# Performance work log

Measured on AMD Instinct MI355X. Metric: run time of the kernel, lower is better.

The kernel has to match this reference:

```python
import jax, jax.numpy as jnp
import numpy as np

BN_EPS = 1e-5
ITER_N = 5

def _bn(x, gamma, beta, mean, var, axis):
    shape = [1] * x.ndim
    shape[axis] = -1
    r = lambda v: v.reshape(shape)
    return (x - r(mean)) * (r(gamma) / jnp.sqrt(r(var) + BN_EPS)) + r(beta)

def _covpool(x):
    # x: (B, d, M); MPNCOV CovpoolLayer: y = x @ I_hat @ x^T, I_hat = (1/M)I - (1/M^2)11^T
    M = x.shape[-1]
    I_hat = (-1.0 / (M * M)) * jnp.ones((M, M), x.dtype) + (1.0 / M) * jnp.eye(M, dtype=x.dtype)
    return jnp.einsum('bdm,mn,ben->bde', x, I_hat, x)

def _sqrtm_ns(A, iterN=ITER_N):
    # MPNCOV SqrtmLayer: trace-normalized Newton-Schulz iteration
    d = A.shape[-1]
    I3 = 3.0 * jnp.eye(d, dtype=A.dtype)
    normA = jnp.trace(A, axis1=1, axis2=2) / 3.0          # (B,)
    A_n = A / normA[:, None, None]
    ZY = 0.5 * (I3 - A_n)
    Y = A_n @ ZY
    Z = ZY
    for _ in range(iterN - 2):
        ZY = 0.5 * (I3 - Z @ Y)
        Y = Y @ ZY
        Z = ZY @ Z
    YZY = 0.5 * (Y @ (I3 - Z @ Y))
    return YZY * jnp.sqrt(normA)[:, None, None]

def setup_inputs() -> dict:
    key = jax.random.key(0)
    ks = jax.random.split(key, 12)
    B, C, H, W = 64, 1024, 16, 16
    D, R = 128, H * W  # att_dim, sp_reso
    return {
        'x': jax.random.normal(ks[0], (B, C, H, W), jnp.float32),
        'w_dr': jax.random.normal(ks[1], (D, C), jnp.float32) * 0.02,
        'b_dr': jax.random.normal(ks[2], (D,), jnp.float32) * 0.02,
        'bn1_gamma': jnp.ones((D,), jnp.float32),
        'bn1_beta': jnp.zeros((D,), jnp.float32),
        'bn1_mean': jax.random.normal(ks[3], (D,), jnp.float32) * 0.1,
        'bn1_var': jax.random.uniform(ks[4], (D,), jnp.float32, 0.5, 1.5),
        'bn2_gamma': jnp.ones((R,), jnp.float32),
        'bn2_beta': jnp.zeros((R,), jnp.float32),
        'bn2_mean': jax.random.normal(ks[5], (R,), jnp.float32) * 0.1,
        'bn2_var': jax.random.uniform(ks[6], (R,), jnp.float32, 0.5, 1.5),
        'rc_w': jax.random.normal(ks[7], (R,), jnp.float32) * 0.1 + 1.0,
        'rc_b': jax.random.normal(ks[8], (R,), jnp.float32) * 0.02,
        'fc_w': jax.random.normal(ks[9], (R, R * R), jnp.float32) * 0.004,
        'fc_b': jax.random.normal(ks[10], (R,), jnp.float32) * 0.02,
    }

def reference(x, w_dr, b_dr, bn1_gamma, bn1_beta, bn1_mean, bn1_var,
              bn2_gamma, bn2_beta, bn2_mean, bn2_var, rc_w, rc_b, fc_w, fc_b):
    B, C, H, W = x.shape
    # 1x1 dimension-reduction conv + BN + ReLU
    y = jnp.einsum('bchw,dc->bdhw', x, w_dr) + b_dr[None, :, None, None]
    y = jax.nn.relu(_bn(y, bn1_gamma, bn1_beta, bn1_mean, bn1_var, axis=1))
    # (B, D, HW) -> (B, HW, D): HW spatial positions as 'channels', D as samples
    y = y.reshape(B, -1, H * W).transpose(0, 2, 1)
    cov = _covpool(y)                  # (B, HW, HW)
    s = _sqrtm_ns(cov, ITER_N)         # (B, HW, HW)
    # row BN over first HW axis (channels of the (B, HW, HW, 1) view)
    s = _bn(s, bn2_gamma, bn2_beta, bn2_mean, bn2_var, axis=1)
    # grouped (depthwise) 1x1 row conv: per-row scale + bias
    s = s * rc_w[None, :, None] + rc_b[None, :, None]
    att = jax.nn.sigmoid(s.reshape(B, -1) @ fc_w.T + fc_b)   # (B, HW)
    att = att.reshape(B, 1, H, W)
    return x * att
```

## Files before the change

### kernel.cpp

```cpp
#include <hip/hip_runtime.h>

typedef unsigned short u16;
typedef unsigned int   u32;
typedef __attribute__((ext_vector_type(8))) short bf8;
typedef __attribute__((ext_vector_type(4))) float f4;
typedef __attribute__((ext_vector_type(16))) float f16f;

#define MFMA(a,b,c)   __builtin_amdgcn_mfma_f32_16x16x32_bf16(a,b,c,0,0,0)
#define MFMA32(a,b,c) __builtin_amdgcn_mfma_f32_32x32x16_bf16(a,b,c,0,0,0)

__device__ __forceinline__ u16 f2bf(float f){
  u32 u = __float_as_uint(f);
  u += 0x7fffu + ((u >> 16) & 1u);
  return (u16)(u >> 16);
}
__device__ __forceinline__ float bf2f(u16 h){ return __uint_as_float(((u32)h) << 16); }
__device__ __forceinline__ u32 pk2(float a, float b){ return (u32)f2bf(a) | ((u32)f2bf(b) << 16); }

__device__ __forceinline__ void glds16(const u16* g, u16* l){
  __builtin_amdgcn_global_load_lds((const __attribute__((address_space(1))) u32*)g,
                                   (__attribute__((address_space(3))) u32*)l, 16, 0, 0);
}

__device__ __forceinline__ bf8 ldsFrag(const char* m, int row0, int k0, int pitch){
  int l = threadIdx.x & 63;
  int r = row0 + (l & 15);
  int kb = ((k0 + ((l >> 4) << 3)) << 1) ^ ((r & 7) << 4);
  return *(const bf8*)(m + r * pitch + kb);
}
__device__ __forceinline__ void ldsPut(char* m, int row, int col, int pitch, u16 v){
  int kb = (col << 1) ^ ((row & 7) << 4);
  *(u16*)(m + row * pitch + kb) = v;
}

__device__ __forceinline__ bf8 fragNS(const char* m, int r0, int ks, int l){
  int r = r0 + (l & 31);
  int kb = ((ks << 5) + ((l >> 5) << 4)) ^ ((r & 15) << 4);
  return *(const bf8*)(m + r * 256 + kb);
}
__device__ __forceinline__ bf8 fragWT(const char* m, int r0, int ks, int l){
  int r = r0 + (l & 31);
  int kb = ((ks << 5) + ((l >> 5) << 4)) ^ ((r & 15) << 4);
  return *(const bf8*)(m + r * 512 + kb);
}
__device__ __forceinline__ char* nsAddr(char* m, int row, int col4){
  return m + row * 256 + ((col4 << 1) ^ ((row & 15) << 4));
}

__device__ __forceinline__ void mmPass(const char* A, const char* B, f16f (&acc)[2][2],
                                       int R0, int C0, int l){
  #pragma unroll
  for (int ks = 0; ks < 8; ++ks){
    bf8 a0 = fragNS(A, R0,      ks, l);
    bf8 a1 = fragNS(A, R0 + 32, ks, l);
    bf8 b0 = fragNS(B, C0,      ks, l);
    bf8 b1 = fragNS(B, C0 + 32, ks, l);
    acc[0][0] = MFMA32(a0, b0, acc[0][0]); acc[0][1] = MFMA32(a0, b1, acc[0][1]);
    acc[1][0] = MFMA32(a1, b0, acc[1][0]); acc[1][1] = MFMA32(a1, b1, acc[1][1]);
  }
}

__device__ __forceinline__ void writeTile(char* D, const f16f (&acc)[2][2], int R0, int C0, int l,
                                          float scale, float dval, const uint2* adv){
  #pragma unroll
  for (int ri = 0; ri < 2; ++ri)
  #pragma unroll
  for (int ci = 0; ci < 2; ++ci)
  #pragma unroll
  for (int g = 0; g < 4; ++g){
    int srow = C0 + ci * 32 + (l & 31);
    int scol = R0 + ri * 32 + g * 8 + ((l >> 5) << 2);
    float v[4];
    #pragma unroll
    for (int q = 0; q < 4; ++q){
      float x = scale * acc[ri][ci][g * 4 + q];
      x += ((scol + q) == srow) ? dval : 0.f;
      v[q] = x;
    }
    if (adv){
      uint2 ad = adv[(ri * 2 + ci) * 4 + g];
      v[0] += 1.5f * bf2f((u16)ad.x);
      v[1] += 1.5f * bf2f((u16)(ad.x >> 16));
      v[2] += 1.5f * bf2f((u16)ad.y);
      v[3] += 1.5f * bf2f((u16)(ad.y >> 16));
    }
    *(uint2*)nsAddr(D, srow, scol) = make_uint2(pk2(v[0], v[1]), pk2(v[2], v[3]));
  }
}

__global__ __launch_bounds__(256) void k_prep(const float* __restrict__ wdr,
                                              float* __restrict__ logits,
                                              u16* __restrict__ prep){
  int i = blockIdx.x * 256 + threadIdx.x;
  if (i < 16384) logits[i] = 0.f;
  #pragma unroll
  for (int j = 0; j < 2; ++j){
    int e = i + j * 65536;
    int chunk = e >> 13, rem = e & 8191, d = rem >> 6, cb2 = rem & 63;
    int c = ((cb2 * 2) ^ ((d & 7) << 4)) >> 1;
    prep[e] = f2bf(wdr[d * 1024 + chunk * 64 + c]);
  }
}

__global__ __launch_bounds__(512) void k_conv(
    const u16* __restrict__ wprep, const float* __restrict__ x, const float* __restrict__ bdr,
    const float* __restrict__ g1, const float* __restrict__ be1,
    const float* __restrict__ m1, const float* __restrict__ v1,
    u16* __restrict__ Wg, u16* __restrict__ WTg){
  __shared__ union {
    struct { u16 A[2][8192]; u16 Bt[2][2048]; } s;
    struct { float y[128 * 33]; float musum[512]; float mu[32]; } e;
  } sm;
  int t = threadIdx.x;
  int b = blockIdx.x >> 3, hw0 = (blockIdx.x & 7) * 32;
  const float* xb = x + (size_t)b * 262144 + hw0;

  int w = t >> 6, l = t & 63;
  int d0 = (w >> 1) * 32, hh = (w & 1) * 16;
  int lc = l & 15, lr = (l >> 4) * 4;

  const f4 fz = {0.f, 0.f, 0.f, 0.f};
  f4 acc[2]; acc[0] = fz; acc[1] = fz;

  int cp = t >> 5, hwl = t & 31;
  int bo0 = (4 * cp) ^ ((hwl & 7) << 4);
  int bo1 = (4 * cp + 64) ^ ((hwl & 7) << 4);

  glds16(wprep + t * 8,        sm.s.A[0] + t * 8);
  glds16(wprep + 4096 + t * 8, sm.s.A[0] + 4096 + t * 8);
  glds16(wprep + 8192 + t * 8,        sm.s.A[1] + t * 8);
  glds16(wprep + 8192 + 4096 + t * 8, sm.s.A[1] + 4096 + t * 8);
  float br0 = xb[(size_t)(2 * cp)      * 256 + hwl];
  float br1 = xb[(size_t)(2 * cp + 1)  * 256 + hwl];
  float br2 = xb[(size_t)(2 * cp + 32) * 256 + hwl];
  float br3 = xb[(size_t)(2 * cp + 33) * 256 + hwl];

  #pragma unroll
  for (int k = 0; k < 16; ++k){
    if (k >= 1 && k < 15){
      const u16* src = wprep + (k + 1) * 8192;
      glds16(src + t * 8,        sm.s.A[(k + 1) & 1] + t * 8);
      glds16(src + 4096 + t * 8, sm.s.A[(k + 1) & 1] + 4096 + t * 8);
    }
    float nb0 = 0.f, nb1 = 0.f, nb2 = 0.f, nb3 = 0.f;
    if (k < 15){
      int c0 = (k + 1) * 64;
      nb0 = xb[(size_t)(c0 + 2 * cp)      * 256 + hwl];
      nb1 = xb[(size_t)(c0 + 2 * cp + 1)  * 256 + hwl];
      nb2 = xb[(size_t)(c0 + 2 * cp + 32) * 256 + hwl];
      nb3 = xb[(size_t)(c0 + 2 * cp + 33) * 256 + hwl];
    }
    __builtin_amdgcn_sched_barrier(0);
    if (k == 0)       asm volatile("s_waitcnt vmcnt(4)" ::: "memory");
    else if (k == 15) asm volatile("s_waitcnt vmcnt(0)" ::: "memory");
    else              asm volatile("s_waitcnt vmcnt(6)" ::: "memory");
    __builtin_amdgcn_sched_barrier(0);
    *(u32*)((char*)sm.s.Bt[k & 1] + hwl * 128 + bo0) = pk2(br0, br1);
    *(u32*)((char*)sm.s.Bt[k & 1] + hwl * 128 + bo1) = pk2(br2, br3);
    asm volatile("s_waitcnt lgkmcnt(0)" ::: "memory");
    __builtin_amdgcn_sched_barrier(0);
    __builtin_amdgcn_s_barrier();
    __builtin_amdgcn_sched_barrier(0);
    #pragma unroll
    for (int ks = 0; ks < 2; ++ks){
      int k0 = ks * 32;
      bf8 a0 = ldsFrag((const char*)sm.s.A[k & 1], d0,      k0, 128);
      bf8 a1 = ldsFrag((const char*)sm.s.A[k & 1], d0 + 16, k0, 128);
      bf8 b0 = ldsFrag((const char*)sm.s.Bt[k & 1], hh, k0, 128);
      acc[0] = MFMA(a0, b0, acc[0]);
      acc[1] = MFMA(a1, b0, acc[1]);
    }
    __builtin_amdgcn_sched_barrier(0);
    __builtin_amdgcn_s_barrier();
    __builtin_amdgcn_sched_barrier(0);
    br0 = nb0; br1 = nb1; br2 = nb2; br3 = nb3;
  }
  __syncthreads();

  #pragma unroll
  for (int i = 0; i < 2; ++i)
    #pragma unroll
    for (int r = 0; r < 4; ++r){
      int d = d0 + i * 16 + lr + r;
      float s1 = g1[d] * rsqrtf(v1[d] + 1e-5f);
      float t1 = (bdr[d] - m1[d]) * s1 + be1[d];
      int hwp = hh + lc;
      sm.e.y[d * 33 + hwp] = fmaxf(acc[i][r] * s1 + t1, 0.f);
    }
  __syncthreads();
  { int part = t >> 5, col = t & 31;
    float s = 0.f;
    #pragma unroll
    for (int i2 = 0; i2 < 8; ++i2) s += sm.e.y[(part * 8 + i2) * 33 + col];
    sm.e.musum[part * 32 + col] = s;
  }
  __syncthreads();
  if (t < 32){
    float m = 0.f;
    #pragma unroll
    for (int p = 0; p < 16; ++p) m += sm.e.musum[p * 32 + t];
    sm.e.mu[t] = m * (1.0f / 128.0f);
  }
  __syncthreads();
  const float ISM = 0.08838834764831845f;
  { int hwp = t >> 4, dc = (t & 15) * 8;
    float muv = sm.e.mu[hwp];
    u32 q[4];
    #pragma unroll
    for (int jj = 0; jj < 4; ++jj){
      float a = (sm.e.y[(dc + 2 * jj)     * 33 + hwp] - muv) * ISM;
      float c = (sm.e.y[(dc + 2 * jj + 1) * 33 + hwp] - muv) * ISM;
      q[jj] = pk2(a, c);
    }
    *(uint4*)(Wg + ((size_t)(b * 256 + hw0 + hwp) * 128 + dc)) = make_uint4(q[0], q[1], q[2], q[3]);
  }
  { int d = t >> 2, hc = (t & 3) * 8;
    u32 q[4];
    #pragma unroll
    for (int jj = 0; jj < 4; ++jj){
      int h0 = hc + 2 * jj, h1 = hc + 2 * jj + 1;
      float a = (sm.e.y[d * 33 + h0] - sm.e.mu[h0]) * ISM;
      float c = (sm.e.y[d * 33 + h1] - sm.e.mu[h1]) * ISM;
      q[jj] = pk2(a, c);
    }
    *(uint4*)(WTg + ((size_t)(b * 128 + d) * 256 + hw0 + hc)) = make_uint4(q[0], q[1], q[2], q[3]);
  }
}

extern __shared__ char smns[];
__global__ __launch_bounds__(512, 2) void k_ns(const u16* __restrict__ WT,
                                               u16* __restrict__ yf, float* __restrict__ normAg){
  int b = blockIdx.x, t = threadIdx.x;
  char* Yb = smns;
  char* Zb = smns + 32768;
  char* T1 = smns + 65536;
  char* T2 = smns + 98304;
  char* T3 = smns + 131072;
  char* WTl = smns + 65536;
  char* G   = T3;
  float* trp = (float*)smns;

  int w = t >> 6, l = t & 63;
  int wq = w & 3;
  int R0 = (wq >> 1) * 64, C0 = (wq & 1) * 64;

  { const u16* src = WT + (size_t)b * 32768;
    int row = t >> 2, q = t & 3;
    #pragma unroll
    for (int j = 0; j < 8; ++j) {
      int c16 = q + j * 4;
      bf8 v = *(const bf8*)(src + row * 256 + c16 * 8);
      int ph = c16 ^ (row & 15);
      *(bf8*)(WTl + row * 512 + ph * 16) = v;
    }
  }
  if (t == 0) *trp = 0.f;
  __syncthreads();

  int R0g = (w & 3) * 32, C0g = (w >> 2) * 64;
  const f16f fz16 = {};
  f16f gac[2]; gac[0] = fz16; gac[1] = fz16;
  #pragma unroll
  for (int ks = 0; ks < 16; ++ks){
    bf8 a  = fragWT(WTl, R0g,      ks, l);
    bf8 b0 = fragWT(WTl, C0g,      ks, l);
    bf8 b1 = fragWT(WTl, C0g + 32, ks, l);
    gac[0] = MFMA32(a, b0, gac[0]);
    gac[1] = MFMA32(a, b1, gac[1]);
  }
  float tp = 0.f;
  #pragma unroll
  for (int ci = 0; ci < 2; ++ci)
    #pragma unroll
    for (int e = 0; e < 16; ++e){
      int row = R0g + (e & 3) + 8 * (e >> 2) + ((l >> 5) << 2);
      int col = C0g + ci * 32 + (l & 31);
      if (row == col) tp += gac[ci][e];
    }
  #pragma unroll
  for (int off = 32; off > 0; off >>= 1) tp += __shfl_down(tp, off);
  if (l == 0) atomicAdd(trp, tp);
  __syncthreads();

  float normA = fmaxf(*trp / 3.0f, 1e-12f);
  if (t == 0) normAg[b] = normA;
  float inv = 1.0f / normA;
  #pragma unroll
  for (int ci = 0; ci < 2; ++ci)
    #pragma unroll
    for (int g = 0; g < 4; ++g){
      int srow = C0g + ci * 32 + (l & 31);
      int scol = R0g + g * 8 + ((l >> 5) << 2);
      float v0 = gac[ci][g * 4 + 0] * inv, v1 = gac[ci][g * 4 + 1] * inv;
      float v2 = gac[ci][g * 4 + 2] * inv, v3 = gac[ci][g * 4 + 3] * inv;
      *(uint2*)nsAddr(G, srow, scol) = make_uint2(pk2(v0, v1), pk2(v2, v3));
    }
  __syncthreads();

  bf8 gA[8], gB[8];
  #pragma unroll
  for (int ks = 0; ks < 8; ++ks){
    gA[ks] = fragNS(G, C0,      ks, l);
    gB[ks] = fragNS(G, C0 + 32, ks, l);
  }
  { int row = t >> 2, q4 = t & 3;
    #pragma unroll
    for (int j = 0; j < 4; ++j){
      int c16 = q4 * 4 + j;
      int ph = c16 ^ (row & 15);
      bf8 gg = *(const bf8*)(G + row * 256 + ph * 16);
      bf8 yv, zv;
      #pragma unroll
      for (int e = 0; e < 8; ++e){
        int col = c16 * 8 + e;
        float y = -0.5f * bf2f((u16)gg[e]) + ((col == row) ? 1.5f : 0.f);
        yv[e] = (short)f2bf(y);
        zv[e] = (col == row) ? (short)f2bf(-0.5f) : (short)0;
      }
      *(bf8*)(Yb + row * 256 + ph * 16) = yv;
      *(bf8*)(Zb + row * 256 + ph * 16) = zv;
    }
  }
  __syncthreads();

  float z0 = 1.5f;
  for (int it = 0; it < 4; ++it){
    {
      f16f acc[2][2]; acc[0][0] = fz16; acc[0][1] = fz16; acc[1][0] = fz16; acc[1][1] = fz16;
      const char* As = (w < 4) ? Zb : Yb;
      #pragma unroll
      for (int ks = 0; ks < 8; ++ks){
        bf8 a0 = fragNS(As, R0,      ks, l);
        bf8 a1 = fragNS(As, R0 + 32, ks, l);
        acc[0][0] = MFMA32(a0, gA[ks], acc[0][0]); acc[0][1] = MFMA32(a0, gB[ks], acc[0][1]);
        acc[1][0] = MFMA32(a1, gA[ks], acc[1][0]); acc[1][1] = MFMA32(a1, gB[ks], acc[1][1]);
      }
      writeTile((w < 4) ? T1 : T3, acc, R0, C0, l, 1.0f, (w < 4) ? z0 : 0.f, nullptr);
    }
    __syncthreads();

    uint2 adv[16];
    {
      const char* addsrc = (w < 4) ? Zb : Yb;
      #pragma unroll
      for (int ri = 0; ri < 2; ++ri)
      #pragma unroll
      for (int ci = 0; ci < 2; ++ci)
      #pragma unroll
      for (int g = 0; g < 4; ++g){
        int srow = C0 + ci * 32 + (l & 31);
        int scol = R0 + ri * 32 + g * 8 + ((l >> 5) << 2);
        adv[(ri * 2 + ci) * 4 + g] = *(const uint2*)nsAddr((char*)addsrc, srow, scol);
      }
      if (w < 4){
        f16f acc[2][2]; acc[0][0] = fz16; acc[0][1] = fz16; acc[1][0] = fz16; acc[1][1] = fz16;
        mmPass(T1, Yb, acc, R0, C0, l);
        writeTile(T2, acc, R0, C0, l, -0.5f, 0.f, nullptr);
      }
    }
    __syncthreads();

    if ((w >= 4) || (it < 3)){
      f16f acc[2][2]; acc[0][0] = fz16; acc[0][1] = fz16; acc[1][0] = fz16; acc[1][1] = fz16;
      const char* A3 = (w < 4) ? T2 : T3;
      const char* B3 = (w < 4) ? T1 : T2;
      mmPass(A3, B3, acc, R0, C0, l);
      writeTile((w < 4) ? Zb : Yb, acc, R0, C0, l, 1.0f, 0.f, adv);
    }
    __syncthreads();
    z0 *= 1.5f;
  }

  { int row = t >> 2, q = t & 3;
    u16* dst = yf + (size_t)b * 16384 + row * 128;
    #pragma unroll
    for (int j = 0; j < 4; ++j) {
      int c16 = q * 4 + j;
      int ph = c16 ^ (row & 15);
      *(bf8*)(dst + c16 * 8) = *(const bf8*)(Yb + row * 256 + ph * 16);
    }
  }
}

extern __shared__ char smex[];
__global__ __launch_bounds__(512) void k_expand(
    const u16* __restrict__ Wg, const u16* __restrict__ yf, const float* __restrict__ normAg,
    const float* __restrict__ g2, const float* __restrict__ be2, const float* __restrict__ m2,
    const float* __restrict__ v2, const float* __restrict__ rcw, const float* __restrict__ rcb,
    u16* __restrict__ sp){
  int blk = blockIdx.x, b = blk >> 2, iband = blk & 3;
  char* Bm = smex;
  char* Yl = smex + 65536;
  char* El = smex + 98304;
  int t = threadIdx.x;
  { const u16* src = Wg + (size_t)b * 32768;
    int row = t >> 1, q = t & 1;
    #pragma unroll
    for (int j = 0; j < 8; ++j) {
      int c16 = q + j * 2;
      bf8 v = *(const bf8*)(src + row * 128 + c16 * 8);
      int ph = c16 ^ (row & 7);
      *(bf8*)(Bm + row * 256 + ph * 16) = v;
    } }
  { const u16* src = yf + (size_t)b * 16384;
    int row = t >> 2, q = t & 3;
    #pragma unroll
    for (int j = 0; j < 4; ++j) {
      int c16 = q + j * 4;
      bf8 v = *(const bf8*)(src + row * 128 + c16 * 8);
      int ph = c16 ^ (row & 7);
      *(bf8*)(Yl + row * 256 + ph * 16) = v;
    } }
  __syncthreads();
  int w = t >> 6, l = t & 63, lc = l & 15, lr = (l >> 4) * 4;
  const f4 fz = {0.f, 0.f, 0.f, 0.f};
  { int r0 = (w >> 2) * 32, c0 = (w & 3) * 32;
    f4 acc[2][2];
    acc[0][0] = fz; acc[0][1] = fz; acc[1][0] = fz; acc[1][1] = fz;
    #pragma unroll
    for (int kk = 0; kk < 4; ++kk) {
      int k0 = kk * 32;
      bf8 a0 = ldsFrag(Bm, iband * 64 + r0,      k0, 256);
      bf8 a1 = ldsFrag(Bm, iband * 64 + r0 + 16, k0, 256);
      bf8 b0 = ldsFrag(Yl, c0,      k0, 256);
      bf8 b1 = ldsFrag(Yl, c0 + 16, k0, 256);
      acc[0][0] = MFMA(a0, b0, acc[0][0]); acc[0][1] = MFMA(a0, b1, acc[0][1]);
      acc[1][0] = MFMA(a1, b0, acc[1][0]); acc[1][1] = MFMA(a1, b1, acc[1][1]);
    }
    #pragma unroll
    for (int i = 0; i < 2; ++i)
      #pragma unroll
      for (int j = 0; j < 2; ++j)
        #pragma unroll
        for (int r = 0; r < 4; ++r)
          ldsPut(El, r0 + i * 16 + lr + r, c0 + j * 16 + lc, 256, f2bf(acc[i][j][r]));
  }
  __syncthreads();
  { float invs = rsqrtf(normAg[b]);
    int r0 = (w >> 2) * 32, c0 = (w & 3) * 64;
    f4 acc[2][4];
    #pragma unroll
    for (int i = 0; i < 2; ++i)
      #pragma unroll
      for (int j = 0; j < 4; ++j) acc[i][j] = fz;
    #pragma unroll
    for (int kk = 0; kk < 4; ++kk) {
      int k0 = kk * 32;
      bf8 a0 = ldsFrag(El, r0,      k0, 256);
      bf8 a1 = ldsFrag(El, r0 + 16, k0, 256);
      bf8 b0 = ldsFrag(Bm, c0,      k0, 256);
      bf8 b1 = ldsFrag(Bm, c0 + 16, k0, 256);
      bf8 b2 = ldsFrag(Bm, c0 + 32, k0, 256);
      bf8 b3 = ldsFrag(Bm, c0 + 48, k0, 256);
      acc[0][0] = MFMA(a0, b0, acc[0][0]); acc[0][1] = MFMA(a0, b1, acc[0][1]);
      acc[0][2] = MFMA(a0, b2, acc[0][2]); acc[0][3] = MFMA(a0, b3, acc[0][3]);
      acc[1][0] = MFMA(a1, b0, acc[1][0]); acc[1][1] = MFMA(a1, b1, acc[1][1]);
      acc[1][2] = MFMA(a1, b2, acc[1][2]); acc[1][3] = MFMA(a1, b3, acc[1][3]);
    }
    #pragma unroll
    for (int i = 0; i < 2; ++i)
      #pragma unroll
      for (int r = 0; r < 4; ++r) {
        int il = r0 + i * 16 + lr + r;
        int ig = iband * 64 + il;
        float bs = g2[ig] * rsqrtf(v2[ig] + 1e-5f);
        float al = bs * rcw[ig];
        float be = (be2[ig] - m2[ig] * bs) * rcw[ig] + rcb[ig];
        #pragma unroll
        for (int j = 0; j < 4; ++j) {
          int jg = c0 + j * 16 + lc;
          sp[(size_t)b * 65536 + ig * 256 + jg] = f2bf(acc[i][j][r] * invs * al + be);
        }
      }
  }
}

__global__ __launch_bounds__(256) void k_fc(const u16* __restrict__ sp,
                                            const float* __restrict__ fcw,
                                            float* __restrict__ partial){
  int kc = blockIdx.x >> 2, rq = blockIdx.x & 3;
  int t = threadIdx.x, w = t >> 6, l = t & 63;
  int k0 = kc * 512;
  int rloc = rq * 64 + w * 16 + (l & 15);
  int kl = k0 + ((l >> 4) << 3);

  const float* bp  = fcw + (size_t)rloc * 65536 + kl;
  const u16*  ap0 = sp + (size_t)((l & 15) +  0) * 65536 + kl;
  const u16*  ap1 = sp + (size_t)((l & 15) + 16) * 65536 + kl;
  const u16*  ap2 = sp + (size_t)((l & 15) + 32) * 65536 + kl;
  const u16*  ap3 = sp + (size_t)((l & 15) + 48) * 65536 + kl;

  const f4 fz = {0.f, 0.f, 0.f, 0.f};
  f4 acc[4]; acc[0] = fz; acc[1] = fz; acc[2] = fz; acc[3] = fz;

  #pragma unroll 4
  for (int ks = 0; ks < 16; ++ks){
    float4 f0 = *(const float4*)(bp + ks * 32);
    float4 f1 = *(const float4*)(bp + ks * 32 + 4);
    union { u32 u[4]; bf8 v; } bb;
    bb.u[0] = (__float_as_uint(f0.x) >> 16) | (__float_as_uint(f0.y) & 0xffff0000u);
    bb.u[1] = (__float_as_uint(f0.z) >> 16) | (__float_as_uint(f0.w) & 0xffff0000u);
    bb.u[2] = (__float_as_uint(f1.x) >> 16) | (__float_as_uint(f1.y) & 0xffff0000u);
    bb.u[3] = (__float_as_uint(f1.z) >> 16) | (__float_as_uint(f1.w) & 0xffff0000u);
    bf8 a0 = *(const bf8*)(ap0 + ks * 32);
    bf8 a1 = *(const bf8*)(ap1 + ks * 32);
    bf8 a2 = *(const bf8*)(ap2 + ks * 32);
    bf8 a3 = *(const bf8*)(ap3 + ks * 32);
    acc[0] = MFMA(a0, bb.v, acc[0]);
    acc[1] = MFMA(a1, bb.v, acc[1]);
    acc[2] = MFMA(a2, bb.v, acc[2]);
    acc[3] = MFMA(a3, bb.v, acc[3]);
  }

  float* pout = partial + (size_t)kc * 16384 + rloc;
  #pragma unroll
  for (int bt = 0; bt < 4; ++bt)
    #pragma unroll
    for (int q = 0; q < 4; ++q){
      int b = bt * 16 + ((l >> 4) << 2) + q;
      pout[b * 256] = acc[bt][q];
    }
}

__global__ __launch_bounds__(64) void k_red(const float* __restrict__ partial,
                                            float* __restrict__ logits){
  int i4 = blockIdx.x * 64 + threadIdx.x;
  const float4* p4 = (const float4*)partial;
  float4 s0 = {0,0,0,0}, s1 = {0,0,0,0}, s2 = {0,0,0,0}, s3 = {0,0,0,0};
  #pragma unroll 8
  for (int kc = 0; kc < 128; kc += 4){
    float4 a = p4[(size_t)(kc + 0) * 4096 + i4];
    float4 b = p4[(size_t)(kc + 1) * 4096 + i4];
    float4 c = p4[(size_t)(kc + 2) * 4096 + i4];
    float4 d = p4[(size_t)(kc + 3) * 4096 + i4];
    s0.x += a.x; s0.y += a.y; s0.z += a.z; s0.w += a.w;
    s1.x += b.x; s1.y += b.y; s1.z += b.z; s1.w += b.w;
    s2.x += c.x; s2.y += c.y; s2.z += c.z; s2.w += c.w;
    s3.x += d.x; s3.y += d.y; s3.z += d.z; s3.w += d.w;
  }
  float4 s;
  s.x = (s0.x + s1.x) + (s2.x + s3.x);
  s.y = (s0.y + s1.y) + (s2.y + s3.y);
  s.z = (s0.z + s1.z) + (s2.z + s3.z);
  s.w = (s0.w + s1.w) + (s2.w + s3.w);
  ((float4*)logits)[i4] = s;
}

__global__ __launch_bounds__(256) void k_mul(const float* __restrict__ x,
                                             const float* __restrict__ logits,
                                             const float* __restrict__ fcb,
                                             float* __restrict__ out, int n4){
  int i = blockIdx.x * 256 + threadIdx.x;
  int str = gridDim.x * 256;
  for (; i < n4; i += str) {
    int e = i << 2;
    int b = e >> 18;
    int hw = e & 255;
    float4 xv = ((const float4*)x)[i];
    float4 lg = *(const float4*)(logits + (b << 8) + hw);
    float4 fb = *(const float4*)(fcb + hw);
    float4 o;
    o.x = xv.x / (1.f + expf(-(lg.x + fb.x)));
    o.y = xv.y / (1.f + expf(-(lg.y + fb.y)));
    o.z = xv.z / (1.f + expf(-(lg.z + fb.z)));
    o.w = xv.w / (1.f + expf(-(lg.w + fb.w)));
    ((float4*)out)[i] = o;
  }
}

extern "C" void kernel_launch(void* const* d_in, const int* in_sizes, int n_in,
                              void* d_out, int out_size, void* d_ws, size_t ws_size,
                              hipStream_t stream){
  const float* x   = (const float*)d_in[0];
  const float* wdr = (const float*)d_in[1];
  const float* bdr = (const float*)d_in[2];
  const float* g1  = (const float*)d_in[3];
  const float* be1 = (const float*)d_in[4];
  const float* m1  = (const float*)d_in[5];
  const float* v1  = (const float*)d_in[6];
  const float* g2  = (const float*)d_in[7];
  const float* be2 = (const float*)d_in[8];
  const float* m2  = (const float*)d_in[9];
  const float* v2  = (const float*)d_in[10];
  const float* rcw = (const float*)d_in[11];
  const float* rcb = (const float*)d_in[12];
  const float* fcw = (const float*)d_in[13];
  const float* fcb = (const float*)d_in[14];
  float* out = (float*)d_out;
  char* ws = (char*)d_ws;
  u16*   Wg  = (u16*)(ws);
  u16*   WTg = (u16*)(ws + (4u  << 20));
  u16*   yfg = (u16*)(ws + (8u  << 20));
  float* nAg = (float*)(ws + (10u << 20));
  u16*   wpr = (u16*)(ws + (10u << 20) + 4096);
  u16*   spg = (u16*)(ws + (11u << 20));
  float* lgt = (float*)(ws + (20u << 20));
  float* prt = (float*)(ws + (24u << 20));

  hipFuncSetAttribute((const void*)k_ns,     hipFuncAttributeMaxDynamicSharedMemorySize, 163840);
  hipFuncSetAttribute((const void*)k_expand, hipFuncAttributeMaxDynamicSharedMemorySize, 114688);

  k_prep  <<<256,  256, 0,      stream>>>(wdr, lgt, wpr);
  k_conv  <<<512,  512, 0,      stream>>>(wpr, x, bdr, g1, be1, m1, v1, Wg, WTg);
  k_ns    <<<64,   512, 163840, stream>>>(WTg, yfg, nAg);
  k_expand<<<256,  512, 114688, stream>>>(Wg, yfg, nAg, g2, be2, m2, v2, rcw, rcb, spg);
  k_fc    <<<512,  256, 0,      stream>>>(spg, fcw, prt);
  k_red   <<<64,   64,  0,      stream>>>(prt, lgt);
  k_mul   <<<2048, 256, 0,      stream>>>(x, lgt, fcb, out, 4194304);
}
```

Baseline: 123.8 us.

## Stage fc weights through double-buffered LDS with 2x2 MFMA tiles in k_fc

The FC kernel now loads the fp32 fc weight tile cooperatively with coalesced row loads, converts it to bf16 with rounding, and writes it into a swizzled, double-buffered LDS tile. Each wave computes a 32x32 output block, so the LDS weight fragments are reused across two batch groups. Global prefetch of the next slice overlaps with the MFMAs via explicit waitcnt and barriers. The reduction kernel is changed to scalar loads with more threads per block. Weight loads should coalesce better, at the cost of LDS traffic and barriers, and weights are now rounded to bf16 rather than truncated.

```diff
diff --git a/kernel.cpp b/kernel.cpp
--- a/kernel.cpp
+++ b/kernel.cpp
@@ -478,72 +478,117 @@
 __global__ __launch_bounds__(256) void k_fc(const u16* __restrict__ sp,
                                             const float* __restrict__ fcw,
                                             float* __restrict__ partial){
+  __shared__ char Bl[2][16384];
   int kc = blockIdx.x >> 2, rq = blockIdx.x & 3;
   int t = threadIdx.x, w = t >> 6, l = t & 63;
-  int k0 = kc * 512;
-  int rloc = rq * 64 + w * 16 + (l & 15);
-  int kl = k0 + ((l >> 4) << 3);
-
-  const float* bp  = fcw + (size_t)rloc * 65536 + kl;
-  const u16*  ap0 = sp + (size_t)((l & 15) +  0) * 65536 + kl;
-  const u16*  ap1 = sp + (size_t)((l & 15) + 16) * 65536 + kl;
-  const u16*  ap2 = sp + (size_t)((l & 15) + 32) * 65536 + kl;
-  const u16*  ap3 = sp + (size_t)((l & 15) + 48) * 65536 + kl;
+  int k0 = kc * 512, rbase = rq * 64;
+  int br0 = (w & 1) * 32;
+  int cr0 = (w >> 1) * 32;
 
   const f4 fz = {0.f, 0.f, 0.f, 0.f};
-  f4 acc[4]; acc[0] = fz; acc[1] = fz; acc[2] = fz; acc[3] = fz;
-
-  #pragma unroll 4
-  for (int ks = 0; ks < 16; ++ks){
-    float4 f0 = *(const float4*)(bp + ks * 32);
-    float4 f1 = *(const float4*)(bp + ks * 32 + 4);
-    union { u32 u[4]; bf8 v; } bb;
-    bb.u[0] = (__float_as_uint(f0.x) >> 16) | (__float_as_uint(f0.y) & 0xffff0000u);
-    bb.u[1] = (__float_as_uint(f0.z) >> 16) | (__float_as_uint(f0.w) & 0xffff0000u);
-    bb.u[2] = (__float_as_uint(f1.x) >> 16) | (__float_as_uint(f1.y) & 0xffff0000u);
-    bb.u[3] = (__float_as_uint(f1.z) >> 16) | (__float_as_uint(f1.w) & 0xffff0000u);
-    bf8 a0 = *(const bf8*)(ap0 + ks * 32);
-    bf8 a1 = *(const bf8*)(ap1 + ks * 32);
-    bf8 a2 = *(const bf8*)(ap2 + ks * 32);
-    bf8 a3 = *(const bf8*)(ap3 + ks * 32);
-    acc[0] = MFMA(a0, bb.v, acc[0]);
-    acc[1] = MFMA(a1, bb.v, acc[1]);
-    acc[2] = MFMA(a2, bb.v, acc[2]);
-    acc[3] = MFMA(a3, bb.v, acc[3]);
-  }
-
-  float* pout = partial + (size_t)kc * 16384 + rloc;
-  #pragma unroll
-  for (int bt = 0; bt < 4; ++bt)
-    #pragma unroll
-    for (int q = 0; q < 4; ++q){
-      int b = bt * 16 + ((l >> 4) << 2) + q;
-      pout[b * 256] = acc[bt][q];
-    }
-}
-
-__global__ __launch_bounds__(64) void k_red(const float* __restrict__ partial,
-                                            float* __restrict__ logits){
-  int i4 = blockIdx.x * 64 + threadIdx.x;
-  const float4* p4 = (const float4*)partial;
-  float4 s0 = {0,0,0,0}, s1 = {0,0,0,0}, s2 = {0,0,0,0}, s3 = {0,0,0,0};
+  f4 acc[2][2];
+  acc[0][0] = fz; acc[0][1] = fz; acc[1][0] = fz; acc[1][1] = fz;
+
+  float4 fbA[8], fbB[8];
+  bf8 faA[8], faB[8];
+
+  #define LOADB(S, FB) { \
+    _Pragma("unroll") \
+    for (int j = 0; j < 8; ++j){ \
+      int fid = t + 256 * j; \
+      int row = fid >> 5, c4 = fid & 31; \
+      FB[j] = *(const float4*)(fcw + (size_t)(rbase + row) * 65536 + k0 + (S) * 128 + c4 * 4); \
+    } }
+  #define LOADA(S, FA) { \
+    _Pragma("unroll") \
+    for (int g = 0; g < 2; ++g) \
+    _Pragma("unroll") \
+    for (int ks = 0; ks < 4; ++ks) \
+      FA[g * 4 + ks] = *(const bf8*)(sp + (size_t)(br0 + 16 * g + (l & 15)) * 65536 \
+                                     + k0 + (S) * 128 + ks * 32 + (l >> 4) * 8); \
+    }
+  #define WRITEB(CUR, FB) { \
+    _Pragma("unroll") \
+    for (int j = 0; j < 8; ++j){ \
+      int fid = t + 256 * j; \
+      int row = fid >> 5, c4 = fid & 31; \
+      int off = row * 256 + ((c4 * 8) ^ ((row & 7) << 4)); \
+      *(uint2*)(&Bl[CUR][0] + off) = make_uint2(pk2(FB[j].x, FB[j].y), pk2(FB[j].z, FB[j].w)); \
+    } }
+  #define DOMFMA(CUR, FA) { \
+    _Pragma("unroll") \
+    for (int ks = 0; ks < 4; ++ks){ \
+      bf8 b0 = ldsFrag(&Bl[CUR][0], cr0,      ks * 32, 256); \
+      bf8 b1 = ldsFrag(&Bl[CUR][0], cr0 + 16, ks * 32, 256); \
+      acc[0][0] = MFMA(FA[ks],     b0, acc[0][0]); \
+      acc[0][1] = MFMA(FA[ks],     b1, acc[0][1]); \
+      acc[1][0] = MFMA(FA[4 + ks], b0, acc[1][0]); \
+      acc[1][1] = MFMA(FA[4 + ks], b1, acc[1][1]); \
+    } }
+  #define FENCE __builtin_amdgcn_sched_barrier(0)
+  #define BARRIER { FENCE; __builtin_amdgcn_s_barrier(); FENCE; }
+
+  LOADB(0, fbA); LOADA(0, faA);
+  LOADB(1, fbB); LOADA(1, faB);
+
+  FENCE; asm volatile("s_waitcnt vmcnt(16)" ::: "memory"); FENCE;
+  WRITEB(0, fbA);
+  asm volatile("s_waitcnt lgkmcnt(0)" ::: "memory");
+  BARRIER;
+  DOMFMA(0, faA);
+  LOADB(2, fbA); LOADA(2, faA);
+  BARRIER;
+  FENCE; asm volatile("s_waitcnt vmcnt(16)" ::: "memory"); FENCE;
+  WRITEB(1, fbB);
+  asm volatile("s_waitcnt lgkmcnt(0)" ::: "memory");
+  BARRIER;
+  DOMFMA(1, faB);
+  LOADB(3, fbB); LOADA(3, faB);
+  BARRIER;
+  FENCE; asm volatile("s_waitcnt vmcnt(16)" ::: "memory"); FENCE;
+  WRITEB(0, fbA);
+  asm volatile("s_waitcnt lgkmcnt(0)" ::: "memory");
+  BARRIER;
+  DOMFMA(0, faA);
+  BARRIER;
+  FENCE; asm volatile("s_waitcnt vmcnt(0)" ::: "memory"); FENCE;
+  WRITEB(1, fbB);
+  asm volatile("s_waitcnt lgkmcnt(0)" ::: "memory");
+  BARRIER;
+  DOMFMA(1, faB);
+
+  #undef LOADB
+  #undef LOADA
+  #undef WRITEB
+  #undef DOMFMA
+  #undef FENCE
+  #undef BARRIER
+
+  float* pout = partial + (size_t)kc * 16384;
+  #pragma unroll
+  for (int g = 0; g < 2; ++g)
+    #pragma unroll
+    for (int j = 0; j < 2; ++j)
+      #pragma unroll
+      for (int q = 0; q < 4; ++q){
+        int brow = br0 + g * 16 + ((l >> 4) << 2) + q;
+        int rcol = rbase + cr0 + j * 16 + (l & 15);
+        pout[brow * 256 + rcol] = acc[g][j][q];
+      }
+}
+
+__global__ __launch_bounds__(256) void k_red(const float* __restrict__ partial,
+                                             float* __restrict__ logits){
+  int i = blockIdx.x * 256 + threadIdx.x;
+  float s0 = 0.f, s1 = 0.f, s2 = 0.f, s3 = 0.f;
   #pragma unroll 8
   for (int kc = 0; kc < 128; kc += 4){
-    float4 a = p4[(size_t)(kc + 0) * 4096 + i4];
-    float4 b = p4[(size_t)(kc + 1) * 4096 + i4];
-    float4 c = p4[(size_t)(kc + 2) * 4096 + i4];
-    float4 d = p4[(size_t)(kc + 3) * 4096 + i4];
-    s0.x += a.x; s0.y += a.y; s0.z += a.z; s0.w += a.w;
-    s1.x += b.x; s1.y += b.y; s1.z += b.z; s1.w += b.w;
-    s2.x += c.x; s2.y += c.y; s2.z += c.z; s2.w += c.w;
-    s3.x += d.x; s3.y += d.y; s3.z += d.z; s3.w += d.w;
-  }
-  float4 s;
-  s.x = (s0.x + s1.x) + (s2.x + s3.x);
-  s.y = (s0.y + s1.y) + (s2.y + s3.y);
-  s.z = (s0.z + s1.z) + (s2.z + s3.z);
-  s.w = (s0.w + s1.w) + (s2.w + s3.w);
-  ((float4*)logits)[i4] = s;
+    s0 += partial[(size_t)(kc + 0) * 16384 + i];
+    s1 += partial[(size_t)(kc + 1) * 16384 + i];
+    s2 += partial[(size_t)(kc + 2) * 16384 + i];
+    s3 += partial[(size_t)(kc + 3) * 16384 + i];
+  }
+  logits[i] = (s0 + s1) + (s2 + s3);
 }
 
 __global__ __launch_bounds__(256) void k_mul(const float* __restrict__ x,
@@ -605,6 +650,6 @@
   k_ns    <<<64,   512, 163840, stream>>>(WTg, yfg, nAg);
   k_expand<<<256,  512, 114688, stream>>>(Wg, yfg, nAg, g2, be2, m2, v2, rcw, rcb, spg);
   k_fc    <<<512,  256, 0,      stream>>>(spg, fcw, prt);
-  k_red   <<<64,   64,  0,      stream>>>(prt, lgt);
+  k_red   <<<64,   256, 0,      stream>>>(prt, lgt);
   k_mul   <<<2048, 256, 0,      stream>>>(x, lgt, fcb, out, 4194304);
 }
```

Measured after the change: 115.3 us. 6.9% less time.
